# Performance work log

Hardware: AMD Instinct MI355X
Metric: run time of the kernel (lower is better)

Reference implementation:

```python
import jax, jax.numpy as jnp
import numpy as np

N_NODES = 20000
N_PATHS = 100000
D_IN = 128
H = 128
N_GRAPHS = 128
N_CLASSES = 10
EPS = 1e-5


def _bn(x, g, b):
    # BatchNorm1d in training mode: biased batch statistics
    m = x.mean(0)
    v = x.var(0)
    return g * (x - m) * jax.lax.rsqrt(v + EPS) + b


def _lstm_final_h(seq, w_ih, w_hh, b_ih, b_hh):
    # seq: [N, T, H] -> final hidden state [N, H]; torch gate order i,f,g,o
    N = seq.shape[0]
    Hd = w_hh.shape[1]
    xg = jnp.einsum('nti,gi->ntg', seq, w_ih) + b_ih + b_hh  # [N, T, 4H]

    def step(carry, g_t):
        h, c = carry
        g = g_t + h @ w_hh.T
        i, f, gg, o = jnp.split(g, 4, axis=-1)
        c = jax.nn.sigmoid(f) * c + jax.nn.sigmoid(i) * jnp.tanh(gg)
        h = jax.nn.sigmoid(o) * jnp.tanh(c)
        return (h, c), None

    init = (jnp.zeros((N, Hd), seq.dtype), jnp.zeros((N, Hd), seq.dtype))
    (h, _), _ = jax.lax.scan(step, init, jnp.swapaxes(xg, 0, 1))
    return h


def setup_inputs() -> dict:
    key = jax.random.key(0)
    ks = jax.random.split(key, 24)
    s = 0.05
    inp = {
        'x': jax.random.normal(ks[0], (N_NODES, D_IN), jnp.float32),
        'path_2': jax.random.randint(ks[1], (N_PATHS, 2), 0, N_NODES),
        'path_3': jax.random.randint(ks[2], (N_PATHS, 3), 0, N_NODES),
        'batch': jnp.sort(jax.random.randint(ks[3], (N_NODES,), 0, N_GRAPHS)),
        # feature encoder: Linear -> BN -> ReLU -> Linear -> BN -> ReLU
        'fe_w1': jax.random.normal(ks[4], (H, D_IN)) * s,
        'fe_b1': jnp.zeros((H,)),
        'fe_g1': jnp.ones((H,)),
        'fe_be1': jnp.zeros((H,)),
        'fe_w2': jax.random.normal(ks[5], (H, H)) * s,
        'fe_b2': jnp.zeros((H,)),
        'fe_g2': jnp.ones((H,)),
        'fe_be2': jnp.zeros((H,)),
        # shared single-layer LSTM (input H -> hidden H)
        'w_ih': jax.random.normal(ks[6], (4 * H, H)) * s,
        'w_hh': jax.random.normal(ks[7], (4 * H, H)) * s,
        'b_ih': jnp.zeros((4 * H,)),
        'b_hh': jnp.zeros((4 * H,)),
        # per-conv batch norms (cutoff-1 = 2 layers)
        'bn1_g': jnp.ones((H,)),
        'bn1_b': jnp.zeros((H,)),
        'bn2_g': jnp.ones((H,)),
        'bn2_b': jnp.zeros((H,)),
        # readout
        'lin1_w': jax.random.normal(ks[8], (H, H)) * s,
        'lin1_b': jnp.zeros((H,)),
        'lin2_w': jax.random.normal(ks[9], (N_CLASSES, H)) * s,
        'lin2_b': jnp.zeros((N_CLASSES,)),
    }
    return inp


def reference(x, path_2, path_3, batch,
              fe_w1, fe_b1, fe_g1, fe_be1, fe_w2, fe_b2, fe_g2, fe_be2,
              w_ih, w_hh, b_ih, b_hh,
              bn1_g, bn1_b, bn2_g, bn2_b,
              lin1_w, lin1_b, lin2_w, lin2_b):
    # feature encoder
    h = jax.nn.relu(_bn(x @ fe_w1.T + fe_b1, fe_g1, fe_be1))
    h = jax.nn.relu(_bn(h @ fe_w2.T + fe_b2, fe_g2, fe_be2))
    # PathConv layers: gather paths -> shared LSTM -> scatter-add -> residual+BN+ReLU
    for paths, bg, bb in ((path_2, bn1_g, bn1_b), (path_3, bn2_g, bn2_b)):
        seq = h[paths]                                   # [n_paths, T, H]
        hf = _lstm_final_h(seq, w_ih, w_hh, b_ih, b_hh)  # [n_paths, H]
        agg = jax.ops.segment_sum(hf, paths[:, -1], num_segments=h.shape[0])
        h = jax.nn.relu(_bn(agg + h, bg, bb))
    # global add pool + MLP head
    pooled = jax.ops.segment_sum(h, batch, num_segments=N_GRAPHS)
    out = jax.nn.relu(pooled @ lin1_w.T + lin1_b)
    return out @ lin2_w.T + lin2_b
```

## Files before the change

### kernel.cpp

```cpp
#include <hip/hip_runtime.h>
#include <cmath>

#define NN 20000
#define NP 100000
#define D  128
#define G4 512
#define NG 128
#define NC 10
#define CHUNK 20000

__device__ __forceinline__ float sigf(float x) { return 1.0f / (1.0f + expf(-x)); }

__global__ __launch_bounds__(256) void gemm_k128(
    const float* __restrict__ A, const float* __restrict__ W,
    const float* __restrict__ bias, float* __restrict__ C,
    int M, int N, int relu)
{
  __shared__ float As[64][129];
  __shared__ float Ws[64][129];
  const int tid = threadIdx.x;
  const int bm = blockIdx.x * 64;
  const int bn = blockIdx.y * 64;

#pragma unroll
  for (int pass = 0; pass < 8; ++pass) {
    int r  = pass * 8 + (tid >> 5);
    int c4 = (tid & 31) * 4;
    float4 va = make_float4(0.f, 0.f, 0.f, 0.f);
    int ga = bm + r;
    if (ga < M) va = *(const float4*)(A + (size_t)ga * 128 + c4);
    As[r][c4 + 0] = va.x; As[r][c4 + 1] = va.y; As[r][c4 + 2] = va.z; As[r][c4 + 3] = va.w;
    float4 vw = make_float4(0.f, 0.f, 0.f, 0.f);
    int gw = bn + r;
    if (gw < N) vw = *(const float4*)(W + (size_t)gw * 128 + c4);
    Ws[r][c4 + 0] = vw.x; Ws[r][c4 + 1] = vw.y; Ws[r][c4 + 2] = vw.z; Ws[r][c4 + 3] = vw.w;
  }
  __syncthreads();

  const int tm = (tid >> 4) * 4;
  const int tn = (tid & 15) * 4;
  float acc[4][4] = {};

#pragma unroll 8
  for (int k = 0; k < 128; ++k) {
    float a0 = As[tm + 0][k], a1 = As[tm + 1][k], a2 = As[tm + 2][k], a3 = As[tm + 3][k];
    float w0 = Ws[tn + 0][k], w1 = Ws[tn + 1][k], w2 = Ws[tn + 2][k], w3 = Ws[tn + 3][k];
    acc[0][0] += a0 * w0; acc[0][1] += a0 * w1; acc[0][2] += a0 * w2; acc[0][3] += a0 * w3;
    acc[1][0] += a1 * w0; acc[1][1] += a1 * w1; acc[1][2] += a1 * w2; acc[1][3] += a1 * w3;
    acc[2][0] += a2 * w0; acc[2][1] += a2 * w1; acc[2][2] += a2 * w2; acc[2][3] += a2 * w3;
    acc[3][0] += a3 * w0; acc[3][1] += a3 * w1; acc[3][2] += a3 * w2; acc[3][3] += a3 * w3;
  }

#pragma unroll
  for (int i = 0; i < 4; ++i) {
    int r = bm + tm + i;
    if (r >= M) continue;
#pragma unroll
    for (int j = 0; j < 4; ++j) {
      int cn = bn + tn + j;
      if (cn >= N) continue;
      float v = acc[i][j] + (bias ? bias[cn] : 0.f);
      if (relu) v = fmaxf(v, 0.f);
      C[(size_t)r * N + cn] = v;
    }
  }
}

__global__ void zero_kernel(float* p, int n) {
  for (int i = blockIdx.x * blockDim.x + threadIdx.x; i < n; i += gridDim.x * blockDim.x)
    p[i] = 0.f;
}

__global__ void addvec_kernel(const float* a, const float* b, float* o, int n) {
  int i = blockIdx.x * blockDim.x + threadIdx.x;
  if (i < n) o[i] = a[i] + b[i];
}

__global__ __launch_bounds__(256) void bn_stats(const float* __restrict__ u,
                                                float* __restrict__ stats,
                                                int M, int rowsPerBlock) {
  __shared__ float sh[512];
  const int j = threadIdx.x & 127;
  const int half = threadIdx.x >> 7;
  int r0 = blockIdx.x * rowsPerBlock;
  int r1 = min(M, r0 + rowsPerBlock);
  float s = 0.f, q = 0.f;
  for (int r = r0 + half; r < r1; r += 2) {
    float v = u[(size_t)r * 128 + j];
    s += v; q += v * v;
  }
  sh[threadIdx.x] = s;
  sh[256 + threadIdx.x] = q;
  __syncthreads();
  if (threadIdx.x < 128) {
    atomicAdd(&stats[j], sh[j] + sh[j + 128]);
    atomicAdd(&stats[128 + j], sh[256 + j] + sh[256 + j + 128]);
  }
}

__global__ void bn_apply_relu(const float* __restrict__ u, const float* __restrict__ stats,
                              const float* __restrict__ g, const float* __restrict__ b,
                              float* __restrict__ out, int n, float invM) {
  int idx = blockIdx.x * blockDim.x + threadIdx.x;
  if (idx >= n) return;
  int j = idx & 127;
  float m = stats[j] * invM;
  float var = stats[128 + j] * invM - m * m;
  float y = g[j] * (u[idx] - m) * rsqrtf(var + 1e-5f) + b[j];
  out[idx] = fmaxf(y, 0.f);
}

__global__ void lstm_step0(const float* __restrict__ Z, float* __restrict__ H1,
                           float* __restrict__ C1, int n) {
  int idx = blockIdx.x * blockDim.x + threadIdx.x;
  if (idx >= n) return;
  int v = idx >> 7, j = idx & 127;
  const float* z = Z + (size_t)v * G4;
  float gi = z[j], gg = z[256 + j], go = z[384 + j];
  float c = sigf(gi) * tanhf(gg);
  float h = sigf(go) * tanhf(c);
  C1[idx] = c;
  H1[idx] = h;
}

__global__ void lstm_final2(const int* __restrict__ path, const float* __restrict__ Z,
                            const float* __restrict__ R1, const float* __restrict__ C1,
                            float* __restrict__ agg, int n) {
  int idx = blockIdx.x * blockDim.x + threadIdx.x;
  if (idx >= n) return;
  int p = idx >> 7, j = idx & 127;
  int a = path[p * 2 + 0], b = path[p * 2 + 1];
  const float* z = Z + (size_t)b * G4;
  const float* r = R1 + (size_t)a * G4;
  float gi = z[j] + r[j];
  float gf = z[128 + j] + r[128 + j];
  float gg = z[256 + j] + r[256 + j];
  float go = z[384 + j] + r[384 + j];
  float c = sigf(gf) * C1[(size_t)a * 128 + j] + sigf(gi) * tanhf(gg);
  float hf = sigf(go) * tanhf(c);
  atomicAdd(&agg[(size_t)b * 128 + j], hf);
}

__global__ void lstm_step1(const int* __restrict__ path, const float* __restrict__ Z,
                           const float* __restrict__ R1, const float* __restrict__ C1,
                           float* __restrict__ h2, float* __restrict__ c2, int n) {
  int idx = blockIdx.x * blockDim.x + threadIdx.x;
  if (idx >= n) return;
  int p = idx >> 7, j = idx & 127;
  int a = path[p * 3 + 0], b = path[p * 3 + 1];
  const float* z = Z + (size_t)b * G4;
  const float* r = R1 + (size_t)a * G4;
  float gi = z[j] + r[j];
  float gf = z[128 + j] + r[128 + j];
  float gg = z[256 + j] + r[256 + j];
  float go = z[384 + j] + r[384 + j];
  float c = sigf(gf) * C1[(size_t)a * 128 + j] + sigf(gi) * tanhf(gg);
  float h = sigf(go) * tanhf(c);
  c2[idx] = c;
  h2[idx] = h;
}

__global__ void lstm_final3(const int* __restrict__ path, const float* __restrict__ Z,
                            const float* __restrict__ R2, const float* __restrict__ c2,
                            float* __restrict__ agg, int n) {
  int idx = blockIdx.x * blockDim.x + threadIdx.x;
  if (idx >= n) return;
  int p = idx >> 7, j = idx & 127;
  int cnode = path[p * 3 + 2];
  const float* z = Z + (size_t)cnode * G4;
  const float* r = R2 + (size_t)p * G4;
  float gi = z[j] + r[j];
  float gf = z[128 + j] + r[128 + j];
  float gg = z[256 + j] + r[256 + j];
  float go = z[384 + j] + r[384 + j];
  float c = sigf(gf) * c2[idx] + sigf(gi) * tanhf(gg);
  float hf = sigf(go) * tanhf(c);
  atomicAdd(&agg[(size_t)cnode * 128 + j], hf);
}

__global__ void pool_kernel(const float* __restrict__ h, const int* __restrict__ batch,
                            float* __restrict__ pooled, int n) {
  int idx = blockIdx.x * blockDim.x + threadIdx.x;
  if (idx >= n) return;
  int v = idx >> 7, j = idx & 127;
  atomicAdd(&pooled[(size_t)batch[v] * 128 + j], h[idx]);
}

extern "C" void kernel_launch(void* const* d_in, const int* in_sizes, int n_in,
                              void* d_out, int out_size, void* d_ws, size_t ws_size,
                              hipStream_t stream) {
  const float* x      = (const float*)d_in[0];
  const int*   path2  = (const int*)d_in[1];
  const int*   path3  = (const int*)d_in[2];
  const int*   batch  = (const int*)d_in[3];
  const float* fe_w1  = (const float*)d_in[4];
  const float* fe_b1  = (const float*)d_in[5];
  const float* fe_g1  = (const float*)d_in[6];
  const float* fe_be1 = (const float*)d_in[7];
  const float* fe_w2  = (const float*)d_in[8];
  const float* fe_b2  = (const float*)d_in[9];
  const float* fe_g2  = (const float*)d_in[10];
  const float* fe_be2 = (const float*)d_in[11];
  const float* w_ih   = (const float*)d_in[12];
  const float* w_hh   = (const float*)d_in[13];
  const float* b_ih   = (const float*)d_in[14];
  const float* b_hh   = (const float*)d_in[15];
  const float* bn1_g  = (const float*)d_in[16];
  const float* bn1_b  = (const float*)d_in[17];
  const float* bn2_g  = (const float*)d_in[18];
  const float* bn2_b  = (const float*)d_in[19];
  const float* lin1_w = (const float*)d_in[20];
  const float* lin1_b = (const float*)d_in[21];
  const float* lin2_w = (const float*)d_in[22];
  const float* lin2_b = (const float*)d_in[23];
  float* out = (float*)d_out;

  float* w = (float*)d_ws;
  float* h    = w; w += (size_t)NN * D;
  float* agg  = w; w += (size_t)NN * D;
  float* Z    = w; w += (size_t)NN * G4;
  float* R1   = w; w += (size_t)NN * G4;
  float* H1   = w; w += (size_t)NN * D;
  float* C1   = w; w += (size_t)NN * D;
  float* h2c  = w; w += (size_t)CHUNK * D;
  float* c2c  = w; w += (size_t)CHUNK * D;
  float* R2c  = w; w += (size_t)CHUNK * G4;
  float* stats  = w; w += 256;
  float* pooled = w; w += (size_t)NG * D;
  float* out1   = w; w += (size_t)NG * D;
  float* bcomb  = w; w += G4;
  float* ency = Z;

  auto gemm = [&](const float* A, const float* Wm, const float* bias, float* Cm,
                  int M, int N, bool relu) {
    dim3 g((M + 63) / 64, (N + 63) / 64);
    gemm_k128<<<g, 256, 0, stream>>>(A, Wm, bias, Cm, M, N, relu ? 1 : 0);
  };
  auto bn = [&](const float* u, const float* gamma, const float* beta, float* o, int M) {
    zero_kernel<<<1, 256, 0, stream>>>(stats, 256);
    const int blocks = 160;
    int rows = (M + blocks - 1) / blocks;
    bn_stats<<<blocks, 256, 0, stream>>>(u, stats, M, rows);
    int n = M * D;
    bn_apply_relu<<<(n + 255) / 256, 256, 0, stream>>>(u, stats, gamma, beta, o, n, 1.0f / M);
  };

  addvec_kernel<<<2, 256, 0, stream>>>(b_ih, b_hh, bcomb, G4);

  gemm(x, fe_w1, fe_b1, ency, NN, D, false);
  bn(ency, fe_g1, fe_be1, h, NN);
  gemm(h, fe_w2, fe_b2, ency, NN, D, false);
  bn(ency, fe_g2, fe_be2, h, NN);

  gemm(h, w_ih, bcomb, Z, NN, G4, false);
  lstm_step0<<<(NN * D + 255) / 256, 256, 0, stream>>>(Z, H1, C1, NN * D);
  gemm(H1, w_hh, nullptr, R1, NN, G4, false);
  hipMemcpyAsync(agg, h, (size_t)NN * D * sizeof(float), hipMemcpyDeviceToDevice, stream);
  lstm_final2<<<(NP * D + 255) / 256, 256, 0, stream>>>(path2, Z, R1, C1, agg, NP * D);
  bn(agg, bn1_g, bn1_b, h, NN);

  gemm(h, w_ih, bcomb, Z, NN, G4, false);
  lstm_step0<<<(NN * D + 255) / 256, 256, 0, stream>>>(Z, H1, C1, NN * D);
  gemm(H1, w_hh, nullptr, R1, NN, G4, false);
  hipMemcpyAsync(agg, h, (size_t)NN * D * sizeof(float), hipMemcpyDeviceToDevice, stream);
  for (int p0 = 0; p0 < NP; p0 += CHUNK) {
    int pc = NP - p0 < CHUNK ? NP - p0 : CHUNK;
    int n = pc * D;
    lstm_step1<<<(n + 255) / 256, 256, 0, stream>>>(path3 + (size_t)p0 * 3, Z, R1, C1,
                                                    h2c, c2c, n);
    gemm(h2c, w_hh, nullptr, R2c, pc, G4, false);
    lstm_final3<<<(n + 255) / 256, 256, 0, stream>>>(path3 + (size_t)p0 * 3, Z, R2c, c2c,
                                                     agg, n);
  }
  bn(agg, bn2_g, bn2_b, h, NN);

  zero_kernel<<<64, 256, 0, stream>>>(pooled, NG * D);
  pool_kernel<<<(NN * D + 255) / 256, 256, 0, stream>>>(h, batch, pooled, NN * D);
  gemm(pooled, lin1_w, lin1_b, out1, NG, D, true);
  gemm(out1, lin2_w, lin2_b, out, NG, NC, false);
}
```

Baseline: 1.252 ms.

## Use 128x128 register-tiled GEMM with swizzled LDS and float4 elementwise kernels

The GEMM moves from 64x64 tiles with 4x4 per-thread outputs to 128x128 tiles with 8x8 per-thread outputs. It stages K in two halves through XOR-swizzled float4 shared memory, prefetching the second half into registers while the first is computed. The LSTM gate, BN apply and pool kernels are vectorised to float4 loads, with each thread handling four features. The larger tiles are meant to raise arithmetic intensity and cut LDS traffic. In exchange they use more registers and give fewer blocks for small M or N, such as the 10-wide head and the N=128 layers.

```diff
diff --git a/kernel.cpp b/kernel.cpp
--- a/kernel.cpp
+++ b/kernel.cpp
@@ -11,52 +11,106 @@
 
 __device__ __forceinline__ float sigf(float x) { return 1.0f / (1.0f + expf(-x)); }
 
-__global__ __launch_bounds__(256) void gemm_k128(
+__global__ __launch_bounds__(256) void gemm128(
     const float* __restrict__ A, const float* __restrict__ W,
     const float* __restrict__ bias, float* __restrict__ C,
     int M, int N, int relu)
 {
-  __shared__ float As[64][129];
-  __shared__ float Ws[64][129];
+  __shared__ float4 As4[2048];
+  __shared__ float4 Ws4[2048];
+
   const int tid = threadIdx.x;
-  const int bm = blockIdx.x * 64;
-  const int bn = blockIdx.y * 64;
+  const int bm = blockIdx.x * 128;
+  const int bn = blockIdx.y * 128;
+
+  const int ty = tid >> 4;
+  const int tx = tid & 15;
+  const int tm = ty * 8;
+  const int tn = tx * 8;
+  const int axor = ty & 7;
+  const int wxor = tx & 7;
+
+  const int sr = tid >> 4;
+  const int sc = tid & 15;
 
 #pragma unroll
   for (int pass = 0; pass < 8; ++pass) {
-    int r  = pass * 8 + (tid >> 5);
-    int c4 = (tid & 31) * 4;
-    float4 va = make_float4(0.f, 0.f, 0.f, 0.f);
-    int ga = bm + r;
-    if (ga < M) va = *(const float4*)(A + (size_t)ga * 128 + c4);
-    As[r][c4 + 0] = va.x; As[r][c4 + 1] = va.y; As[r][c4 + 2] = va.z; As[r][c4 + 3] = va.w;
-    float4 vw = make_float4(0.f, 0.f, 0.f, 0.f);
-    int gw = bn + r;
-    if (gw < N) vw = *(const float4*)(W + (size_t)gw * 128 + c4);
-    Ws[r][c4 + 0] = vw.x; Ws[r][c4 + 1] = vw.y; Ws[r][c4 + 2] = vw.z; Ws[r][c4 + 3] = vw.w;
-  }
+    int r = pass * 16 + sr;
+    int sw = sc ^ ((r >> 3) & 7);
+    int ga = bm + r; ga = ga < M ? ga : M - 1;
+    As4[r * 16 + sw] = *(const float4*)(A + (size_t)ga * 128 + sc * 4);
+    int gw = bn + r; gw = gw < N ? gw : N - 1;
+    Ws4[r * 16 + sw] = *(const float4*)(W + (size_t)gw * 128 + sc * 4);
+  }
+
+  float4 pa[8], pw[8];
+#pragma unroll
+  for (int pass = 0; pass < 8; ++pass) {
+    int r = pass * 16 + sr;
+    int ga = bm + r; ga = ga < M ? ga : M - 1;
+    pa[pass] = *(const float4*)(A + (size_t)ga * 128 + 64 + sc * 4);
+    int gw = bn + r; gw = gw < N ? gw : N - 1;
+    pw[pass] = *(const float4*)(W + (size_t)gw * 128 + 64 + sc * 4);
+  }
+
+  float acc[8][8] = {};
+
   __syncthreads();
 
-  const int tm = (tid >> 4) * 4;
-  const int tn = (tid & 15) * 4;
-  float acc[4][4] = {};
-
-#pragma unroll 8
-  for (int k = 0; k < 128; ++k) {
-    float a0 = As[tm + 0][k], a1 = As[tm + 1][k], a2 = As[tm + 2][k], a3 = As[tm + 3][k];
-    float w0 = Ws[tn + 0][k], w1 = Ws[tn + 1][k], w2 = Ws[tn + 2][k], w3 = Ws[tn + 3][k];
-    acc[0][0] += a0 * w0; acc[0][1] += a0 * w1; acc[0][2] += a0 * w2; acc[0][3] += a0 * w3;
-    acc[1][0] += a1 * w0; acc[1][1] += a1 * w1; acc[1][2] += a1 * w2; acc[1][3] += a1 * w3;
-    acc[2][0] += a2 * w0; acc[2][1] += a2 * w1; acc[2][2] += a2 * w2; acc[2][3] += a2 * w3;
-    acc[3][0] += a3 * w0; acc[3][1] += a3 * w1; acc[3][2] += a3 * w2; acc[3][3] += a3 * w3;
-  }
-
-#pragma unroll
-  for (int i = 0; i < 4; ++i) {
+#pragma unroll 2
+  for (int k4 = 0; k4 < 16; ++k4) {
+    float4 av[8], wv[8];
+#pragma unroll
+    for (int i = 0; i < 8; ++i) av[i] = As4[(tm + i) * 16 + (k4 ^ axor)];
+#pragma unroll
+    for (int j = 0; j < 8; ++j) wv[j] = Ws4[(tn + j) * 16 + (k4 ^ wxor)];
+#pragma unroll
+    for (int i = 0; i < 8; ++i)
+#pragma unroll
+      for (int j = 0; j < 8; ++j) {
+        acc[i][j] = fmaf(av[i].x, wv[j].x, acc[i][j]);
+        acc[i][j] = fmaf(av[i].y, wv[j].y, acc[i][j]);
+        acc[i][j] = fmaf(av[i].z, wv[j].z, acc[i][j]);
+        acc[i][j] = fmaf(av[i].w, wv[j].w, acc[i][j]);
+      }
+  }
+
+  __syncthreads();
+
+#pragma unroll
+  for (int pass = 0; pass < 8; ++pass) {
+    int r = pass * 16 + sr;
+    int sw = sc ^ ((r >> 3) & 7);
+    As4[r * 16 + sw] = pa[pass];
+    Ws4[r * 16 + sw] = pw[pass];
+  }
+
+  __syncthreads();
+
+#pragma unroll 2
+  for (int k4 = 0; k4 < 16; ++k4) {
+    float4 av[8], wv[8];
+#pragma unroll
+    for (int i = 0; i < 8; ++i) av[i] = As4[(tm + i) * 16 + (k4 ^ axor)];
+#pragma unroll
+    for (int j = 0; j < 8; ++j) wv[j] = Ws4[(tn + j) * 16 + (k4 ^ wxor)];
+#pragma unroll
+    for (int i = 0; i < 8; ++i)
+#pragma unroll
+      for (int j = 0; j < 8; ++j) {
+        acc[i][j] = fmaf(av[i].x, wv[j].x, acc[i][j]);
+        acc[i][j] = fmaf(av[i].y, wv[j].y, acc[i][j]);
+        acc[i][j] = fmaf(av[i].z, wv[j].z, acc[i][j]);
+        acc[i][j] = fmaf(av[i].w, wv[j].w, acc[i][j]);
+      }
+  }
+
+#pragma unroll
+  for (int i = 0; i < 8; ++i) {
     int r = bm + tm + i;
     if (r >= M) continue;
 #pragma unroll
-    for (int j = 0; j < 4; ++j) {
+    for (int j = 0; j < 8; ++j) {
       int cn = bn + tn + j;
       if (cn >= N) continue;
       float v = acc[i][j] + (bias ? bias[cn] : 0.f);
@@ -100,90 +154,129 @@
 
 __global__ void bn_apply_relu(const float* __restrict__ u, const float* __restrict__ stats,
                               const float* __restrict__ g, const float* __restrict__ b,
-                              float* __restrict__ out, int n, float invM) {
-  int idx = blockIdx.x * blockDim.x + threadIdx.x;
-  if (idx >= n) return;
-  int j = idx & 127;
-  float m = stats[j] * invM;
-  float var = stats[128 + j] * invM - m * m;
-  float y = g[j] * (u[idx] - m) * rsqrtf(var + 1e-5f) + b[j];
-  out[idx] = fmaxf(y, 0.f);
+                              float* __restrict__ out, int n4, float invM) {
+  int idx = blockIdx.x * blockDim.x + threadIdx.x;
+  if (idx >= n4) return;
+  int q = idx & 31;
+  float4 uv = ((const float4*)u)[idx];
+  float4 sv = ((const float4*)stats)[q];
+  float4 qv = ((const float4*)stats)[32 + q];
+  float4 gv = ((const float4*)g)[q];
+  float4 bv = ((const float4*)b)[q];
+  float4 o;
+  {
+    float m = sv.x * invM, var = qv.x * invM - m * m;
+    o.x = fmaxf(gv.x * (uv.x - m) * rsqrtf(var + 1e-5f) + bv.x, 0.f);
+  }
+  {
+    float m = sv.y * invM, var = qv.y * invM - m * m;
+    o.y = fmaxf(gv.y * (uv.y - m) * rsqrtf(var + 1e-5f) + bv.y, 0.f);
+  }
+  {
+    float m = sv.z * invM, var = qv.z * invM - m * m;
+    o.z = fmaxf(gv.z * (uv.z - m) * rsqrtf(var + 1e-5f) + bv.z, 0.f);
+  }
+  {
+    float m = sv.w * invM, var = qv.w * invM - m * m;
+    o.w = fmaxf(gv.w * (uv.w - m) * rsqrtf(var + 1e-5f) + bv.w, 0.f);
+  }
+  ((float4*)out)[idx] = o;
 }
 
 __global__ void lstm_step0(const float* __restrict__ Z, float* __restrict__ H1,
-                           float* __restrict__ C1, int n) {
-  int idx = blockIdx.x * blockDim.x + threadIdx.x;
-  if (idx >= n) return;
-  int v = idx >> 7, j = idx & 127;
-  const float* z = Z + (size_t)v * G4;
-  float gi = z[j], gg = z[256 + j], go = z[384 + j];
-  float c = sigf(gi) * tanhf(gg);
-  float h = sigf(go) * tanhf(c);
-  C1[idx] = c;
-  H1[idx] = h;
+                           float* __restrict__ C1, int n4) {
+  int idx = blockIdx.x * blockDim.x + threadIdx.x;
+  if (idx >= n4) return;
+  int v = idx >> 5, q = idx & 31;
+  const float4* z = (const float4*)(Z + (size_t)v * G4);
+  float4 zi = z[q], zg = z[64 + q], zo = z[96 + q];
+  float4 c, h;
+  c.x = sigf(zi.x) * tanhf(zg.x); h.x = sigf(zo.x) * tanhf(c.x);
+  c.y = sigf(zi.y) * tanhf(zg.y); h.y = sigf(zo.y) * tanhf(c.y);
+  c.z = sigf(zi.z) * tanhf(zg.z); h.z = sigf(zo.z) * tanhf(c.z);
+  c.w = sigf(zi.w) * tanhf(zg.w); h.w = sigf(zo.w) * tanhf(c.w);
+  ((float4*)C1)[idx] = c;
+  ((float4*)H1)[idx] = h;
+}
+
+__device__ __forceinline__ void lstm_gate4(const float4 zi, const float4 zf,
+                                           const float4 zg, const float4 zo,
+                                           const float4 ri, const float4 rf,
+                                           const float4 rg, const float4 ro,
+                                           const float4 cin, float4* cout, float4* hout) {
+  float c, out;
+  c = sigf(zf.x + rf.x) * cin.x + sigf(zi.x + ri.x) * tanhf(zg.x + rg.x);
+  out = sigf(zo.x + ro.x) * tanhf(c); cout->x = c; hout->x = out;
+  c = sigf(zf.y + rf.y) * cin.y + sigf(zi.y + ri.y) * tanhf(zg.y + rg.y);
+  out = sigf(zo.y + ro.y) * tanhf(c); cout->y = c; hout->y = out;
+  c = sigf(zf.z + rf.z) * cin.z + sigf(zi.z + ri.z) * tanhf(zg.z + rg.z);
+  out = sigf(zo.z + ro.z) * tanhf(c); cout->z = c; hout->z = out;
+  c = sigf(zf.w + rf.w) * cin.w + sigf(zi.w + ri.w) * tanhf(zg.w + rg.w);
+  out = sigf(zo.w + ro.w) * tanhf(c); cout->w = c; hout->w = out;
 }
 
 __global__ void lstm_final2(const int* __restrict__ path, const float* __restrict__ Z,
                             const float* __restrict__ R1, const float* __restrict__ C1,
-                            float* __restrict__ agg, int n) {
-  int idx = blockIdx.x * blockDim.x + threadIdx.x;
-  if (idx >= n) return;
-  int p = idx >> 7, j = idx & 127;
+                            float* __restrict__ agg, int n4) {
+  int idx = blockIdx.x * blockDim.x + threadIdx.x;
+  if (idx >= n4) return;
+  int p = idx >> 5, q = idx & 31;
   int a = path[p * 2 + 0], b = path[p * 2 + 1];
-  const float* z = Z + (size_t)b * G4;
-  const float* r = R1 + (size_t)a * G4;
-  float gi = z[j] + r[j];
-  float gf = z[128 + j] + r[128 + j];
-  float gg = z[256 + j] + r[256 + j];
-  float go = z[384 + j] + r[384 + j];
-  float c = sigf(gf) * C1[(size_t)a * 128 + j] + sigf(gi) * tanhf(gg);
-  float hf = sigf(go) * tanhf(c);
-  atomicAdd(&agg[(size_t)b * 128 + j], hf);
+  const float4* z = (const float4*)(Z + (size_t)b * G4);
+  const float4* r = (const float4*)(R1 + (size_t)a * G4);
+  float4 cin = ((const float4*)(C1 + (size_t)a * D))[q];
+  float4 c, h;
+  lstm_gate4(z[q], z[32 + q], z[64 + q], z[96 + q],
+             r[q], r[32 + q], r[64 + q], r[96 + q], cin, &c, &h);
+  float* dst = agg + (size_t)b * D + q * 4;
+  atomicAdd(dst + 0, h.x); atomicAdd(dst + 1, h.y);
+  atomicAdd(dst + 2, h.z); atomicAdd(dst + 3, h.w);
 }
 
 __global__ void lstm_step1(const int* __restrict__ path, const float* __restrict__ Z,
                            const float* __restrict__ R1, const float* __restrict__ C1,
-                           float* __restrict__ h2, float* __restrict__ c2, int n) {
-  int idx = blockIdx.x * blockDim.x + threadIdx.x;
-  if (idx >= n) return;
-  int p = idx >> 7, j = idx & 127;
+                           float* __restrict__ h2, float* __restrict__ c2, int n4) {
+  int idx = blockIdx.x * blockDim.x + threadIdx.x;
+  if (idx >= n4) return;
+  int p = idx >> 5, q = idx & 31;
   int a = path[p * 3 + 0], b = path[p * 3 + 1];
-  const float* z = Z + (size_t)b * G4;
-  const float* r = R1 + (size_t)a * G4;
-  float gi = z[j] + r[j];
-  float gf = z[128 + j] + r[128 + j];
-  float gg = z[256 + j] + r[256 + j];
-  float go = z[384 + j] + r[384 + j];
-  float c = sigf(gf) * C1[(size_t)a * 128 + j] + sigf(gi) * tanhf(gg);
-  float h = sigf(go) * tanhf(c);
-  c2[idx] = c;
-  h2[idx] = h;
+  const float4* z = (const float4*)(Z + (size_t)b * G4);
+  const float4* r = (const float4*)(R1 + (size_t)a * G4);
+  float4 cin = ((const float4*)(C1 + (size_t)a * D))[q];
+  float4 c, h;
+  lstm_gate4(z[q], z[32 + q], z[64 + q], z[96 + q],
+             r[q], r[32 + q], r[64 + q], r[96 + q], cin, &c, &h);
+  ((float4*)c2)[idx] = c;
+  ((float4*)h2)[idx] = h;
 }
 
 __global__ void lstm_final3(const int* __restrict__ path, const float* __restrict__ Z,
                             const float* __restrict__ R2, const float* __restrict__ c2,
-                            float* __restrict__ agg, int n) {
-  int idx = blockIdx.x * blockDim.x + threadIdx.x;
-  if (idx >= n) return;
-  int p = idx >> 7, j = idx & 127;
+                            float* __restrict__ agg, int n4) {
+  int idx = blockIdx.x * blockDim.x + threadIdx.x;
+  if (idx >= n4) return;
+  int p = idx >> 5, q = idx & 31;
   int cnode = path[p * 3 + 2];
-  const float* z = Z + (size_t)cnode * G4;
-  const float* r = R2 + (size_t)p * G4;
-  float gi = z[j] + r[j];
-  float gf = z[128 + j] + r[128 + j];
-  float gg = z[256 + j] + r[256 + j];
-  float go = z[384 + j] + r[384 + j];
-  float c = sigf(gf) * c2[idx] + sigf(gi) * tanhf(gg);
-  float hf = sigf(go) * tanhf(c);
-  atomicAdd(&agg[(size_t)cnode * 128 + j], hf);
+  const float4* z = (const float4*)(Z + (size_t)cnode * G4);
+  const float4* r = (const float4*)(R2 + (size_t)p * G4);
+  float4 cin = ((const float4*)c2)[idx];
+  float4 c, h;
+  lstm_gate4(z[q], z[32 + q], z[64 + q], z[96 + q],
+             r[q], r[32 + q], r[64 + q], r[96 + q], cin, &c, &h);
+  float* dst = agg + (size_t)cnode * D + q * 4;
+  atomicAdd(dst + 0, h.x); atomicAdd(dst + 1, h.y);
+  atomicAdd(dst + 2, h.z); atomicAdd(dst + 3, h.w);
 }
 
 __global__ void pool_kernel(const float* __restrict__ h, const int* __restrict__ batch,
-                            float* __restrict__ pooled, int n) {
-  int idx = blockIdx.x * blockDim.x + threadIdx.x;
-  if (idx >= n) return;
-  int v = idx >> 7, j = idx & 127;
-  atomicAdd(&pooled[(size_t)batch[v] * 128 + j], h[idx]);
+                            float* __restrict__ pooled, int n4) {
+  int idx = blockIdx.x * blockDim.x + threadIdx.x;
+  if (idx >= n4) return;
+  int v = idx >> 5, q = idx & 31;
+  float4 hv = ((const float4*)h)[idx];
+  float* dst = pooled + (size_t)batch[v] * D + q * 4;
+  atomicAdd(dst + 0, hv.x); atomicAdd(dst + 1, hv.y);
+  atomicAdd(dst + 2, hv.z); atomicAdd(dst + 3, hv.w);
 }
 
 extern "C" void kernel_launch(void* const* d_in, const int* in_sizes, int n_in,
@@ -233,16 +326,16 @@
 
   auto gemm = [&](const float* A, const float* Wm, const float* bias, float* Cm,
                   int M, int N, bool relu) {
-    dim3 g((M + 63) / 64, (N + 63) / 64);
-    gemm_k128<<<g, 256, 0, stream>>>(A, Wm, bias, Cm, M, N, relu ? 1 : 0);
+    dim3 g((M + 127) / 128, (N + 127) / 128);
+    gemm128<<<g, 256, 0, stream>>>(A, Wm, bias, Cm, M, N, relu ? 1 : 0);
   };
   auto bn = [&](const float* u, const float* gamma, const float* beta, float* o, int M) {
     zero_kernel<<<1, 256, 0, stream>>>(stats, 256);
     const int blocks = 160;
     int rows = (M + blocks - 1) / blocks;
     bn_stats<<<blocks, 256, 0, stream>>>(u, stats, M, rows);
-    int n = M * D;
-    bn_apply_relu<<<(n + 255) / 256, 256, 0, stream>>>(u, stats, gamma, beta, o, n, 1.0f / M);
+    int n4 = M * 32;
+    bn_apply_relu<<<(n4 + 255) / 256, 256, 0, stream>>>(u, stats, gamma, beta, o, n4, 1.0f / M);
   };
 
   addvec_kernel<<<2, 256, 0, stream>>>(b_ih, b_hh, bcomb, G4);
@@ -253,29 +346,29 @@
   bn(ency, fe_g2, fe_be2, h, NN);
 
   gemm(h, w_ih, bcomb, Z, NN, G4, false);
-  lstm_step0<<<(NN * D + 255) / 256, 256, 0, stream>>>(Z, H1, C1, NN * D);
+  lstm_step0<<<(NN * 32 + 255) / 256, 256, 0, stream>>>(Z, H1, C1, NN * 32);
   gemm(H1, w_hh, nullptr, R1, NN, G4, false);
   hipMemcpyAsync(agg, h, (size_t)NN * D * sizeof(float), hipMemcpyDeviceToDevice, stream);
-  lstm_final2<<<(NP * D + 255) / 256, 256, 0, stream>>>(path2, Z, R1, C1, agg, NP * D);
+  lstm_final2<<<(NP * 32 + 255) / 256, 256, 0, stream>>>(path2, Z, R1, C1, agg, NP * 32);
   bn(agg, bn1_g, bn1_b, h, NN);
 
   gemm(h, w_ih, bcomb, Z, NN, G4, false);
-  lstm_step0<<<(NN * D + 255) / 256, 256, 0, stream>>>(Z, H1, C1, NN * D);
+  lstm_step0<<<(NN * 32 + 255) / 256, 256, 0, stream>>>(Z, H1, C1, NN * 32);
   gemm(H1, w_hh, nullptr, R1, NN, G4, false);
   hipMemcpyAsync(agg, h, (size_t)NN * D * sizeof(float), hipMemcpyDeviceToDevice, stream);
   for (int p0 = 0; p0 < NP; p0 += CHUNK) {
     int pc = NP - p0 < CHUNK ? NP - p0 : CHUNK;
-    int n = pc * D;
-    lstm_step1<<<(n + 255) / 256, 256, 0, stream>>>(path3 + (size_t)p0 * 3, Z, R1, C1,
-                                                    h2c, c2c, n);
+    int n4 = pc * 32;
+    lstm_step1<<<(n4 + 255) / 256, 256, 0, stream>>>(path3 + (size_t)p0 * 3, Z, R1, C1,
+                                                     h2c, c2c, n4);
     gemm(h2c, w_hh, nullptr, R2c, pc, G4, false);
-    lstm_final3<<<(n + 255) / 256, 256, 0, stream>>>(path3 + (size_t)p0 * 3, Z, R2c, c2c,
-                                                     agg, n);
+    lstm_final3<<<(n4 + 255) / 256, 256, 0, stream>>>(path3 + (size_t)p0 * 3, Z, R2c, c2c,
+                                                      agg, n4);
   }
   bn(agg, bn2_g, bn2_b, h, NN);
 
   zero_kernel<<<64, 256, 0, stream>>>(pooled, NG * D);
-  pool_kernel<<<(NN * D + 255) / 256, 256, 0, stream>>>(h, batch, pooled, NN * D);
+  pool_kernel<<<(NN * 32 + 255) / 256, 256, 0, stream>>>(h, batch, pooled, NN * 32);
   gemm(pooled, lin1_w, lin1_b, out1, NG, D, true);
   gemm(out1, lin2_w, lin2_b, out, NG, NC, false);
 }
```

Result: slower. 1.580 ms (+26.2%).
